# Performance work log

Hardware: AMD Instinct MI355X
Metric: run time of the kernel (lower is better)

The kernel has to match this reference:

```python
import jax, jax.numpy as jnp
import numpy as np

B, N, C = 4, 4096, 128
IK, CK = 9, 9  # inner_k, cross_k
BN_EPS = 1e-5


def setup_inputs() -> dict:
    key = jax.random.key(0)
    ks = jax.random.split(key, 8)
    d = {}
    d["x"] = jax.random.normal(ks[0], (B, N, C), jnp.float32)
    d["y"] = jax.random.normal(ks[1], (B, N, C), jnp.float32)
    d["x_mask"] = jnp.ones((B, N), jnp.float32)
    d["y_mask"] = jnp.ones((B, N), jnp.float32)
    specs = [("mr0", C, 2 * C), ("mr1", C, 2 * C), ("fc", C, C), ("f1", 4 * C, C), ("f2", C, 4 * C)]
    for (name, o, i), k in zip(specs, jax.random.split(ks[2], len(specs))):
        d[name + "_W"] = jax.random.normal(k, (o, i), jnp.float32) * 0.05
        d[name + "_b"] = jnp.zeros((o,), jnp.float32)
        d[name + "_g"] = jnp.ones((o,), jnp.float32)
        d[name + "_beta"] = jnp.zeros((o,), jnp.float32)
        d[name + "_m"] = jnp.zeros((o,), jnp.float32)
        d[name + "_v"] = jnp.ones((o,), jnp.float32)
    return d


def _sqdist(a, b):
    # a: [B,Na,C], b: [B,Nb,C] -> [B,Na,Nb]
    return (jnp.sum(a * a, -1)[:, :, None] + jnp.sum(b * b, -1)[:, None, :]
            - 2.0 * jnp.einsum('bnc,bmc->bnm', a, b))


def _knn(x, y):
    # neighbor indices into concat([x;y]) for every node: [B, Nx+Ny, IK+CK]
    Nx = x.shape[1]
    i_xx = jax.lax.top_k(-_sqdist(x, x), IK)[1]
    i_xy = jax.lax.top_k(-_sqdist(x, y), CK)[1] + Nx
    i_yy = jax.lax.top_k(-_sqdist(y, y), IK)[1] + Nx
    i_yx = jax.lax.top_k(-_sqdist(y, x), CK)[1]
    return jnp.concatenate([jnp.concatenate([i_xx, i_xy], -1),
                            jnp.concatenate([i_yy, i_yx], -1)], axis=1)


def _bn(h, g, b, m, v):
    # eval-mode BatchNorm over channel (last) axis
    return (h - m) * jax.lax.rsqrt(v + BN_EPS) * g + b


def _gelu(h):
    return jax.nn.gelu(h, approximate=False)


def _mrconv(f, nbr, W, b, g, be, m, v):
    # f: [B,Nt,C], nbr: [B,Nt,K] -> Conv(2C->C)+BN+GELU of interleaved [x, max_j(x_j-x_i)]
    xj = jax.vmap(lambda fb, nb: fb[nb])(f, nbr)          # [B,Nt,K,C] gather
    msg = jnp.max(xj - f[:, :, None, :], axis=2)          # [B,Nt,C]
    Bh, Nt, Ch = f.shape
    h = jnp.stack([f, msg], axis=-1).reshape(Bh, Nt, 2 * Ch)  # channel interleave as in torch reshape
    h = jnp.einsum('bnc,oc->bno', h, W) + b
    return _gelu(_bn(h, g, be, m, v))


def _forward(x, x_mask, y, y_mask,
             mr0_W, mr0_b, mr0_g, mr0_beta, mr0_m, mr0_v,
             mr1_W, mr1_b, mr1_g, mr1_beta, mr1_m, mr1_v,
             fc_W, fc_b, fc_g, fc_beta, fc_m, fc_v,
             f1_W, f1_b, f1_g, f1_beta, f1_m, f1_v,
             f2_W, f2_b, f2_g, f2_beta, f2_m, f2_v):
    Nx = x.shape[1]
    nbr = _knn(x, y)
    xy = jnp.concatenate([x, y], axis=1)
    xy = _mrconv(xy, nbr, mr0_W, mr0_b, mr0_g, mr0_beta, mr0_m, mr0_v) + xy
    xy = _mrconv(xy, nbr, mr1_W, mr1_b, mr1_g, mr1_beta, mr1_m, mr1_v) + xy
    xg, yg = xy[:, :Nx], xy[:, Nx:]

    def fc(h):
        return _bn(jnp.einsum('bnc,oc->bno', h, fc_W) + fc_b, fc_g, fc_beta, fc_m, fc_v)

    xo = fc(xg) + x
    yo = fc(yg) + y

    def ffn(h):
        r = h
        h = _gelu(_bn(jnp.einsum('bnc,oc->bno', h, f1_W) + f1_b, f1_g, f1_beta, f1_m, f1_v))
        h = _gelu(_bn(jnp.einsum('bnc,oc->bno', h, f2_W) + f2_b, f2_g, f2_beta, f2_m, f2_v))
        return h + r

    xo = ffn(xo) * x_mask[:, :, None]
    yo = ffn(yo) * y_mask[:, :, None]
    return xo, yo


def reference(x, x_mask, y, y_mask,
              mr0_W, mr0_b, mr0_g, mr0_beta, mr0_m, mr0_v,
              mr1_W, mr1_b, mr1_g, mr1_beta, mr1_m, mr1_v,
              fc_W, fc_b, fc_g, fc_beta, fc_m, fc_v,
              f1_W, f1_b, f1_g, f1_beta, f1_m, f1_v,
              f2_W, f2_b, f2_g, f2_beta, f2_m, f2_v):
    return _forward(x, x_mask, y, y_mask,
                    mr0_W, mr0_b, mr0_g, mr0_beta, mr0_m, mr0_v,
                    mr1_W, mr1_b, mr1_g, mr1_beta, mr1_m, mr1_v,
                    fc_W, fc_b, fc_g, fc_beta, fc_m, fc_v,
                    f1_W, f1_b, f1_g, f1_beta, f1_m, f1_v,
                    f2_W, f2_b, f2_g, f2_beta, f2_m, f2_v)
```

## Files before the change

### kernel.cpp

```cpp
#include <hip/hip_runtime.h>
#include <hip/hip_bf16.h>
#include <float.h>
#include <math.h>

#define BB 4
#define N1 4096
#define NT 8192
#define CH 128
#define NBRS 18
#define ZSEL 2.35f
#define LCAP 40
#define EQ 4096.0f
#define GQGAP 6
#define GQCOV 3

typedef __attribute__((ext_vector_type(8))) short s16x8;
typedef __attribute__((ext_vector_type(16))) float f32x16;
typedef __attribute__((ext_vector_type(4))) float f32x4;

__device__ inline unsigned short f2bf(float v) {
  unsigned u = __float_as_uint(v);
  unsigned r = (u + 0x7FFFu + ((u >> 16) & 1u)) >> 16;
  return (unsigned short)r;
}
__device__ inline float bf2f(unsigned short h) {
  return __uint_as_float((unsigned)h << 16);
}
__device__ inline unsigned mapf(float f) {
  unsigned u = __float_as_uint(f);
  return (u & 0x80000000u) ? ~u : (u | 0x80000000u);
}
__device__ inline float gelu_f(float x) {
  return 0.5f * x * (1.0f + erff(x * 0.70710678118654752f));
}

__global__ __launch_bounds__(256) void wsplit_k(const float* __restrict__ w,
                                                unsigned short* __restrict__ hi,
                                                unsigned short* __restrict__ lo,
                                                int n) {
  int t = blockIdx.x * 256 + threadIdx.x;
  if (t < n) {
    float v = w[t];
    unsigned short h = f2bf(v);
    float r = v - bf2f(h);
    hi[t] = h; lo[t] = f2bf(r);
  }
}

__global__ __launch_bounds__(256) void norms_concat_k(const float* __restrict__ x,
                                                      const float* __restrict__ y,
                                                      float* __restrict__ xy,
                                                      float* __restrict__ norms) {
  int w = (blockIdx.x * 256 + threadIdx.x) >> 6;
  int lane = threadIdx.x & 63;
  int b = w >> 13, row = w & 8191;
  const float* src = (row < N1) ? (x + ((size_t)b * N1 + row) * CH)
                                : (y + ((size_t)b * N1 + (row - N1)) * CH);
  float2 v = *(const float2*)(src + lane * 2);
  *(float2*)(xy + (size_t)w * CH + lane * 2) = v;
  float s = v.x * v.x + v.y * v.y;
  for (int off = 32; off > 0; off >>= 1) s += __shfl_down(s, off);
  if (lane == 0) norms[w] = s;
}

__global__ __launch_bounds__(256) void cbt_k(const float* __restrict__ xy,
                                             unsigned short* __restrict__ cbt) {
  int t = blockIdx.x * 256 + threadIdx.x;
  int u = t >> 15, p = t & 32767;
  const float* src = xy + (size_t)p * CH + u * 8;
  unsigned hw[4], lw[4];
#pragma unroll
  for (int j = 0; j < 4; ++j) {
    float v0 = src[2 * j], v1 = src[2 * j + 1];
    unsigned short h0 = f2bf(v0), h1 = f2bf(v1);
    float r0 = v0 - bf2f(h0);
    float r1 = v1 - bf2f(h1);
    unsigned short l0 = f2bf(r0), l1 = f2bf(r1);
    hw[j] = (unsigned)h0 | ((unsigned)h1 << 16);
    lw[j] = (unsigned)l0 | ((unsigned)l1 << 16);
  }
  *(uint4*)&cbt[((size_t)u * 32768 + p) * 8] = make_uint4(hw[0], hw[1], hw[2], hw[3]);
  *(uint4*)&cbt[((size_t)(u + 16) * 32768 + p) * 8] = make_uint4(lw[0], lw[1], lw[2], lw[3]);
}

__global__ __launch_bounds__(256) void knn4_k(const unsigned short* __restrict__ cbt,
                                              const float* __restrict__ norms,
                                              int* __restrict__ nbr,
                                              int* __restrict__ cntg,
                                              unsigned* __restrict__ listA,
                                              unsigned* __restrict__ listB,
                                              unsigned short* __restrict__ fbl) {
  __shared__ unsigned short __align__(16) cst[2][32][32][8];
  __shared__ float cn_s[2][32];
  __shared__ unsigned lst[128][2][LCAP];
  __shared__ unsigned short lcnt[128][2];
  const int tid = threadIdx.x;
  const int qblk = blockIdx.x, z = blockIdx.y;
  const int b = z >> 2, combo = z & 3;
  const int qoff = (combo <= 1) ? 0 : N1;
  const int coff = (combo == 0 || combo == 3) ? 0 : N1;
  const int w = tid >> 6;
  const int cl = tid & 31;
  const int h = (tid >> 5) & 1;
  const int h4 = 4 * h;
  const int ql = w * 32 + cl;
  const int q = qblk * 128 + ql;
  const size_t qp = (size_t)b * NT + qoff + q;
  const size_t cb0 = (size_t)b * NT + coff;

  const s16x8* cv = (const s16x8*)cbt;
  s16x8 bh[8], bl[8];
#pragma unroll
  for (int s = 0; s < 8; ++s) {
    bh[s] = cv[(size_t)(2 * s + h) * 32768 + qp];
    bl[s] = cv[(size_t)(16 + 2 * s + h) * 32768 + qp];
  }

  const float nq = norms[qp];
  const float Tc = 128.f - ZSEL * sqrtf(256.f + 4.f * nq);
  int cnt = 0;

  const int su = tid >> 5, sc = tid & 31;
  const char* p0 = (const char*)&cbt[((size_t)(su) * 32768 + cb0 + sc) * 8];
  const char* p1 = (const char*)&cbt[((size_t)(8 + su) * 32768 + cb0 + sc) * 8];
  const char* p2 = (const char*)&cbt[((size_t)(16 + su) * 32768 + cb0 + sc) * 8];
  const char* p3 = (const char*)&cbt[((size_t)(24 + su) * 32768 + cb0 + sc) * 8];
  const float* pn = norms + cb0 + tid;

  uint4 st[4]; float cnreg = 0.f;
  st[0] = *(const uint4*)p0; p0 += 512;
  st[1] = *(const uint4*)p1; p1 += 512;
  st[2] = *(const uint4*)p2; p2 += 512;
  st[3] = *(const uint4*)p3; p3 += 512;
  if (tid < 32) { cnreg = *pn; pn += 32; }
  *(uint4*)&cst[0][su][sc][0] = st[0];
  *(uint4*)&cst[0][8 + su][sc][0] = st[1];
  *(uint4*)&cst[0][16 + su][sc][0] = st[2];
  *(uint4*)&cst[0][24 + su][sc][0] = st[3];
  if (tid < 32) cn_s[0][tid] = cnreg;
  __syncthreads();

  int buf = 0;
  for (int t = 0; t < 128; ++t) {
    if (t < 127) {
      st[0] = *(const uint4*)p0; p0 += 512;
      st[1] = *(const uint4*)p1; p1 += 512;
      st[2] = *(const uint4*)p2; p2 += 512;
      st[3] = *(const uint4*)p3; p3 += 512;
      if (tid < 32) { cnreg = *pn; pn += 32; }
    }
    f32x16 acc = {0.f,0.f,0.f,0.f,0.f,0.f,0.f,0.f,0.f,0.f,0.f,0.f,0.f,0.f,0.f,0.f};
#pragma unroll
    for (int s = 0; s < 8; ++s) {
      s16x8 a0 = *(const s16x8*)&cst[buf][2 * s + h][cl][0];
      s16x8 a1 = *(const s16x8*)&cst[buf][16 + 2 * s + h][cl][0];
      acc = __builtin_amdgcn_mfma_f32_32x32x16_bf16(a0, bh[s], acc, 0, 0, 0);
      acc = __builtin_amdgcn_mfma_f32_32x32x16_bf16(a0, bl[s], acc, 0, 0, 0);
      acc = __builtin_amdgcn_mfma_f32_32x32x16_bf16(a1, bh[s], acc, 0, 0, 0);
    }
    float4 c0 = *(const float4*)&cn_s[buf][h4];
    float4 c1 = *(const float4*)&cn_s[buf][8 + h4];
    float4 c2 = *(const float4*)&cn_s[buf][16 + h4];
    float4 c3 = *(const float4*)&cn_s[buf][24 + h4];
    const float cw[16] = {c0.x, c0.y, c0.z, c0.w, c1.x, c1.y, c1.z, c1.w,
                          c2.x, c2.y, c2.z, c2.w, c3.x, c3.y, c3.z, c3.w};
    const int ib = t * 32 + h4;
#pragma unroll
    for (int g = 0; g < 4; ++g) {
#pragma unroll
      for (int rr = 0; rr < 4; ++rr) {
        const int r = g * 4 + rr;
        float s = fmaf(-2.0f, acc[r], cw[r]);
        if (s <= Tc) {
          int e = (int)((Tc - s) * EQ);
          e = e > 0xFFFFF ? 0xFFFFF : e;
          unsigned key = ((unsigned)e << 12) | (unsigned)(4095 - (ib + g * 8 + rr));
          if (cnt < LCAP) lst[ql][h][cnt] = key;
          ++cnt;
        }
      }
    }
    if (t < 127) {
      *(uint4*)&cst[buf ^ 1][su][sc][0] = st[0];
      *(uint4*)&cst[buf ^ 1][8 + su][sc][0] = st[1];
      *(uint4*)&cst[buf ^ 1][16 + su][sc][0] = st[2];
      *(uint4*)&cst[buf ^ 1][24 + su][sc][0] = st[3];
      if (tid < 32) cn_s[buf ^ 1][tid] = cnreg;
    }
    __syncthreads();
    buf ^= 1;
  }
  lcnt[ql][h] = (unsigned short)cnt;
  __syncthreads();

  if (tid < 128) {
    const int mq = tid;
    const int gq = z * 4096 + qblk * 128 + mq;
    const int c0 = lcnt[mq][0], c1 = lcnt[mq][1];
    const bool over = (c0 > LCAP) || (c1 > LCAP);
    const int n0 = c0 > LCAP ? LCAP : c0;
    const int n1 = c1 > LCAP ? LCAP : c1;
    const int m = n0 + n1;
    unsigned top[10];
#pragma unroll
    for (int j = 0; j < 10; ++j) top[j] = 0u;
    for (int li = 0; li < 2; ++li) {
      const int n = li ? n1 : n0;
      for (int i = 0; i < n; ++i) {
        unsigned key = lst[mq][li][i];
        if (key > top[9]) {
#pragma unroll
          for (int j = 0; j < 10; ++j) {
            bool sw = key > top[j];
            unsigned tv = top[j];
            top[j] = sw ? key : tv;
            key = sw ? tv : key;
          }
        }
      }
    }
    const unsigned e8 = top[8] >> 12, e9 = top[9] >> 12;
    const bool cov = !over && (m >= 9) && (e8 >= GQCOV);
    const bool ok = cov && (m == 9 || (e8 - e9) >= GQGAP);
    const int qg = qblk * 128 + mq;
    const int row = (combo <= 1) ? qg : (N1 + qg);
    const int slot = (combo == 0 || combo == 2) ? 0 : 9;
    const int ioff = (combo == 1 || combo == 2) ? N1 : 0;
    int* dst = nbr + ((size_t)b * NT + row) * NBRS + slot;
    if (ok) {
#pragma unroll
      for (int s = 0; s < 9; ++s)
        dst[s] = (int)(4095u - (top[s] & 0xFFFu)) + ioff;
    } else if (!cov || m > 64) {
      int idx = atomicAdd(&cntg[1], 1);
      listB[idx] = (unsigned)gq;
    } else {
      int idx = atomicAdd(&cntg[0], 1);
      listA[idx] = ((unsigned)m << 16) | (unsigned)gq;
      unsigned short* fp = fbl + (size_t)gq * 64;
      int p = 0;
      for (int i = 0; i < n0; ++i) fp[p++] = (unsigned short)(4095u - (lst[mq][0][i] & 0xFFFu));
      for (int i = 0; i < n1; ++i) fp[p++] = (unsigned short)(4095u - (lst[mq][1][i] & 0xFFFu));
    }
  }
}

__global__ __launch_bounds__(256) void rerank_sl_k(const float* __restrict__ xy,
                                                   const float* __restrict__ norms,
                                                   const unsigned short* __restrict__ fbl,
                                                   const unsigned* __restrict__ listA,
                                                   const int* __restrict__ cntg,
                                                   int* __restrict__ nbr) {
  const int lane = threadIdx.x & 63;
  const int wv = threadIdx.x >> 6;
  const int nA = cntg[0];
  for (int i = blockIdx.x * 4 + wv; i < nA; i += gridDim.x * 4) {
    const unsigned ent = listA[i];
    const int gq = (int)(ent & 0xffffu);
    const int m = (int)(ent >> 16);
    const int z = gq >> 12, q = gq & 4095;
    const int b = z >> 2, combo = z & 3;
    const int qoff = (combo <= 1) ? 0 : N1;
    const int coff = (combo == 0 || combo == 3) ? 0 : N1;
    const size_t cq = (size_t)b * NT + coff;
    const int row = (combo <= 1) ? q : (N1 + q);
    const int slot = (combo == 0 || combo == 2) ? 0 : 9;
    const int ioff = (combo == 1 || combo == 2) ? N1 : 0;
    int* dst = nbr + ((size_t)b * NT + row) * NBRS + slot;
    const float* qrow = xy + ((size_t)b * NT + qoff + q) * CH;

    int ci = 0; float de = FLT_MAX;
    if (lane < m) {
      ci = (int)fbl[(size_t)gq * 64 + lane];
      const float* crow = xy + (cq + ci) * CH;
      const float cnv = norms[cq + ci];
      float a0 = 0.f, a1 = 0.f, a2 = 0.f, a3 = 0.f;
#pragma unroll
      for (int k = 0; k < 32; ++k) {
        float4 qv = *(const float4*)(qrow + k * 4);
        float4 cv2 = *(const float4*)(crow + k * 4);
        a0 = fmaf(qv.x, cv2.x, a0); a1 = fmaf(qv.y, cv2.y, a1);
        a2 = fmaf(qv.z, cv2.z, a2); a3 = fmaf(qv.w, cv2.w, a3);
      }
      de = cnv - 2.0f * ((a0 + a1) + (a2 + a3));
    }
    unsigned long long key = ((unsigned long long)mapf(de) << 32) | (unsigned)ci;
    if (lane >= m) key = ~0ull;
    int xr = 0;
#pragma unroll 1
    for (int k = 0; k < m; ++k) {
      unsigned long long kk = __shfl(key, k);
      xr += (kk < key) ? 1 : 0;
    }
    if (lane < m && xr < 9) dst[xr] = ci + ioff;
  }
}

__global__ __launch_bounds__(256) void rerank_fs_k(const float* __restrict__ xy,
                                                   const float* __restrict__ norms,
                                                   const unsigned* __restrict__ listB,
                                                   const int* __restrict__ cntg,
                                                   int* __restrict__ nbr) {
  __shared__ unsigned long long ms[4][576];
  __shared__ unsigned long long wk[36];
  const int tid = threadIdx.x;
  const int lane = tid & 63, wv = tid >> 6;
  const int nB = cntg[1];
  for (int i = blockIdx.x; i < nB; i += gridDim.x) {
    const int gq = (int)listB[i];
    const int z = gq >> 12, q = gq & 4095;
    const int b = z >> 2, combo = z & 3;
    const int qoff = (combo <= 1) ? 0 : N1;
    const int coff = (combo == 0 || combo == 3) ? 0 : N1;
    const size_t cq = (size_t)b * NT + coff;
    const int row = (combo <= 1) ? q : (N1 + q);
    const int slot = (combo == 0 || combo == 2) ? 0 : 9;
    const int ioff = (combo == 1 || combo == 2) ? N1 : 0;
    int* dst = nbr + ((size_t)b * NT + row) * NBRS + slot;
    const float* qrow = xy + ((size_t)b * NT + qoff + q) * CH;

    unsigned long long bl9[9];
#pragma unroll
    for (int j = 0; j < 9; ++j) bl9[j] = ~0ull;
    for (int it = 0; it < 16; ++it) {
      const int cc = (it * 4 + wv) * 64 + lane;
      const float* crow = xy + (cq + cc) * CH;
      float a0 = 0.f, a1 = 0.f, a2 = 0.f, a3 = 0.f;
#pragma unroll
      for (int k = 0; k < 32; ++k) {
        float4 qv = *(const float4*)(qrow + k * 4);
        float4 cv2 = *(const float4*)(crow + k * 4);
        a0 = fmaf(qv.x, cv2.x, a0); a1 = fmaf(qv.y, cv2.y, a1);
        a2 = fmaf(qv.z, cv2.z, a2); a3 = fmaf(qv.w, cv2.w, a3);
      }
      float d2v = norms[cq + cc] - 2.0f * ((a0 + a1) + (a2 + a3));
      unsigned long long key = ((unsigned long long)mapf(d2v) << 32) | (unsigned)cc;
      if (key < bl9[8]) {
#pragma unroll
        for (int jj = 0; jj < 9; ++jj) {
          bool sw = key < bl9[jj];
          unsigned long long tv = bl9[jj];
          bl9[jj] = sw ? key : tv;
          key = sw ? tv : key;
        }
      }
    }
#pragma unroll
    for (int s = 0; s < 9; ++s) ms[wv][lane * 9 + s] = bl9[s];
    int ptr = 0;
    for (int s = 0; s < 9; ++s) {
      unsigned long long hd = ms[wv][lane * 9 + ptr];
      unsigned long long mn = hd;
#pragma unroll
      for (int off = 1; off < 64; off <<= 1) {
        unsigned long long ot = __shfl_xor(mn, off);
        mn = (ot < mn) ? ot : mn;
      }
      unsigned long long wm = __ballot(hd == mn);
      int wl = __ffsll(wm) - 1;
      if (lane == wl) ptr++;
      if (lane == 0) wk[wv * 9 + s] = mn;
    }
    __syncthreads();
    if (wv == 0) {
      unsigned long long key = (lane < 36) ? wk[lane] : ~0ull;
      int xr = 0;
#pragma unroll 1
      for (int k = 0; k < 36; ++k) {
        unsigned long long kk = __shfl(key, k);
        xr += (kk < key) ? 1 : 0;
      }
      if (lane < 36 && xr < 9) dst[xr] = (int)(unsigned)(key & 0xffffffffull) + ioff;
    }
    __syncthreads();
  }
}

__global__ __launch_bounds__(256) void mrconv2_k(const float* __restrict__ in,
                                                 const int* __restrict__ nbr,
                                                 const unsigned short* __restrict__ Whi,
                                                 const unsigned short* __restrict__ Wlo,
                                                 const float* __restrict__ bias,
                                                 const float* __restrict__ gam,
                                                 const float* __restrict__ bet,
                                                 const float* __restrict__ mean,
                                                 const float* __restrict__ var,
                                                 float* __restrict__ out) {
  __shared__ float h[32][260];
  const int tid = threadIdx.x;
  const int pt0 = blockIdx.x * 32;
  {
    const int w = tid >> 6, lane = tid & 63;
    for (int pp = 0; pp < 8; ++pp) {
      const int p = w * 8 + pp;
      const int n = pt0 + p;
      const int b = n >> 13;
      const float* frow = in + (size_t)n * CH;
      float2 f2 = *(const float2*)(frow + lane * 2);
      float mx = -FLT_MAX, my = -FLT_MAX;
      const int* nb = nbr + (size_t)n * NBRS;
      for (int j = 0; j < NBRS; ++j) {
        int idx = nb[j];
        const float* vrow = in + ((size_t)b * NT + idx) * CH;
        float2 v2 = *(const float2*)(vrow + lane * 2);
        mx = fmaxf(mx, v2.x - f2.x);
        my = fmaxf(my, v2.y - f2.y);
      }
      h[p][lane * 4 + 0] = f2.x; h[p][lane * 4 + 1] = mx;
      h[p][lane * 4 + 2] = f2.y; h[p][lane * 4 + 3] = my;
    }
  }
  __syncthreads();
  const int lane = tid & 63, w = tid >> 6;
  const int r16 = lane & 15, kg = lane >> 4;
  f32x4 acc[2][2] = {{{0.f,0.f,0.f,0.f},{0.f,0.f,0.f,0.f}},
                     {{0.f,0.f,0.f,0.f},{0.f,0.f,0.f,0.f}}};
#pragma unroll
  for (int ks = 0; ks < 8; ++ks) {
    s16x8 ah[2], al[2];
#pragma unroll
    for (int rt = 0; rt < 2; ++rt) {
      const float* hp = &h[rt * 16 + r16][(ks * 4 + kg) * 8];
#pragma unroll
      for (int j = 0; j < 8; ++j) {
        float v = hp[j];
        unsigned short hb = f2bf(v);
        float rr = v - bf2f(hb);
        ah[rt][j] = (short)hb;
        al[rt][j] = (short)f2bf(rr);
      }
    }
#pragma unroll
    for (int cbi = 0; cbi < 2; ++cbi) {
      const int o = (w * 2 + cbi) * 16 + r16;
      s16x8 bh2 = *(const s16x8*)(Whi + o * 256 + ks * 32 + kg * 8);
      s16x8 bl2 = *(const s16x8*)(Wlo + o * 256 + ks * 32 + kg * 8);
#pragma unroll
      for (int rt = 0; rt < 2; ++rt) {
        acc[rt][cbi] = __builtin_amdgcn_mfma_f32_16x16x32_bf16(ah[rt], bh2, acc[rt][cbi], 0, 0, 0);
        acc[rt][cbi] = __builtin_amdgcn_mfma_f32_16x16x32_bf16(ah[rt], bl2, acc[rt][cbi], 0, 0, 0);
        acc[rt][cbi] = __builtin_amdgcn_mfma_f32_16x16x32_bf16(al[rt], bh2, acc[rt][cbi], 0, 0, 0);
      }
    }
  }
#pragma unroll
  for (int cbi = 0; cbi < 2; ++cbi) {
    const int o = (w * 2 + cbi) * 16 + r16;
    const float sc = gam[o] / sqrtf(var[o] + 1e-5f);
    const float bs = bias[o], mo = mean[o], be = bet[o];
#pragma unroll
    for (int rt = 0; rt < 2; ++rt) {
#pragma unroll
      for (int rg = 0; rg < 4; ++rg) {
        const int row = rt * 16 + kg * 4 + rg;
        const int n = pt0 + row;
        float bn = (acc[rt][cbi][rg] + bs - mo) * sc + be;
        float gl = gelu_f(bn);
        out[(size_t)n * CH + o] = gl + h[row][2 * o];
      }
    }
  }
}

__global__ __launch_bounds__(256) void fc2_k(const float* __restrict__ in,
                                             const unsigned short* __restrict__ Whi,
                                             const unsigned short* __restrict__ Wlo,
                                             const float* __restrict__ bias,
                                             const float* __restrict__ gam,
                                             const float* __restrict__ bet,
                                             const float* __restrict__ mean,
                                             const float* __restrict__ var,
                                             const float* __restrict__ xres,
                                             const float* __restrict__ yres,
                                             float* __restrict__ out) {
  __shared__ unsigned short __align__(16) aHi[16][16][8];
  __shared__ unsigned short __align__(16) aLo[16][16][8];
  const int tid = threadIdx.x;
  const int pt0 = blockIdx.x * 16;
  {
    const int row = tid >> 4, ku = tid & 15;
    const float* src = in + (size_t)(pt0 + row) * CH + ku * 8;
    unsigned hw[4], lw[4];
#pragma unroll
    for (int j = 0; j < 4; ++j) {
      float v0 = src[2 * j], v1 = src[2 * j + 1];
      unsigned short h0 = f2bf(v0), h1 = f2bf(v1);
      float r0 = v0 - bf2f(h0), r1 = v1 - bf2f(h1);
      hw[j] = (unsigned)h0 | ((unsigned)h1 << 16);
      lw[j] = (unsigned)f2bf(r0) | ((unsigned)f2bf(r1) << 16);
    }
    *(uint4*)&aHi[ku][row][0] = make_uint4(hw[0], hw[1], hw[2], hw[3]);
    *(uint4*)&aLo[ku][row][0] = make_uint4(lw[0], lw[1], lw[2], lw[3]);
  }
  __syncthreads();
  const int lane = tid & 63, w = tid >> 6;
  const int r16 = lane & 15, kg = lane >> 4;
  f32x4 acc[2] = {{0.f,0.f,0.f,0.f}, {0.f,0.f,0.f,0.f}};
#pragma unroll
  for (int ks = 0; ks < 4; ++ks) {
    s16x8 ah = *(const s16x8*)&aHi[ks * 4 + kg][r16][0];
    s16x8 al = *(const s16x8*)&aLo[ks * 4 + kg][r16][0];
#pragma unroll
    for (int cb = 0; cb < 2; ++cb) {
      const int o = w * 32 + cb * 16 + r16;
      s16x8 bh2 = *(const s16x8*)(Whi + o * 128 + ks * 32 + kg * 8);
      s16x8 bl2 = *(const s16x8*)(Wlo + o * 128 + ks * 32 + kg * 8);
      acc[cb] = __builtin_amdgcn_mfma_f32_16x16x32_bf16(ah, bh2, acc[cb], 0, 0, 0);
      acc[cb] = __builtin_amdgcn_mfma_f32_16x16x32_bf16(ah, bl2, acc[cb], 0, 0, 0);
      acc[cb] = __builtin_amdgcn_mfma_f32_16x16x32_bf16(al, bh2, acc[cb], 0, 0, 0);
    }
  }
#pragma unroll
  for (int cb = 0; cb < 2; ++cb) {
    const int o = w * 32 + cb * 16 + r16;
    const float sc = gam[o] / sqrtf(var[o] + 1e-5f);
    const float bs = bias[o], mo = mean[o], be = bet[o];
#pragma unroll
    for (int rg = 0; rg < 4; ++rg) {
      const int row = kg * 4 + rg;
      const int n = pt0 + row;
      const int b = n >> 13, prow = n & 8191;
      float bn = (acc[cb][rg] + bs - mo) * sc + be;
      float res = (prow < N1) ? xres[((size_t)b * N1 + prow) * CH + o]
                              : yres[((size_t)b * N1 + prow - N1) * CH + o];
      out[(size_t)n * CH + o] = bn + res;
    }
  }
}

__global__ __launch_bounds__(256) void ffn2_k(const float* __restrict__ u,
                                              const unsigned short* __restrict__ W1hi,
                                              const unsigned short* __restrict__ W1lo,
                                              const float* __restrict__ b1,
                                              const float* __restrict__ g1,
                                              const float* __restrict__ be1,
                                              const float* __restrict__ m1,
                                              const float* __restrict__ v1,
                                              const unsigned short* __restrict__ W2hi,
                                              const unsigned short* __restrict__ W2lo,
                                              const float* __restrict__ b2,
                                              const float* __restrict__ g2,
                                              const float* __restrict__ be2,
                                              const float* __restrict__ m2,
                                              const float* __restrict__ v2,
                                              const float* __restrict__ xmask,
                                              const float* __restrict__ ymask,
                                              float* __restrict__ outbuf) {
  __shared__ unsigned short __align__(16) aHi[16][16][8];
  __shared__ unsigned short __align__(16) aLo[16][16][8];
  __shared__ unsigned short __align__(16) hHi[64][16][8];
  __shared__ unsigned short __align__(16) hLo[64][16][8];
  const int tid = threadIdx.x;
  const int pt0 = blockIdx.x * 16;
  {
    const int row = tid >> 4, ku = tid & 15;
    const float* src = u + (size_t)(pt0 + row) * CH + ku * 8;
    unsigned hw[4], lw[4];
#pragma unroll
    for (int j = 0; j < 4; ++j) {
      float v0 = src[2 * j], v1 = src[2 * j + 1];
      unsigned short h0 = f2bf(v0), h1 = f2bf(v1);
      float r0 = v0 - bf2f(h0), r1 = v1 - bf2f(h1);
      hw[j] = (unsigned)h0 | ((unsigned)h1 << 16);
      lw[j] = (unsigned)f2bf(r0) | ((unsigned)f2bf(r1) << 16);
    }
    *(uint4*)&aHi[ku][row][0] = make_uint4(hw[0], hw[1], hw[2], hw[3]);
    *(uint4*)&aLo[ku][row][0] = make_uint4(lw[0], lw[1], lw[2], lw[3]);
  }
  __syncthreads();
  const int lane = tid & 63, w = tid >> 6;
  const int r16 = lane & 15, kg = lane >> 4;
  {
    f32x4 acc[8];
#pragma unroll
    for (int cb = 0; cb < 8; ++cb) acc[cb] = {0.f, 0.f, 0.f, 0.f};
#pragma unroll
    for (int ks = 0; ks < 4; ++ks) {
      s16x8 ah = *(const s16x8*)&aHi[ks * 4 + kg][r16][0];
      s16x8 al = *(const s16x8*)&aLo[ks * 4 + kg][r16][0];
#pragma unroll
      for (int cb = 0; cb < 8; ++cb) {
        const int o = w * 128 + cb * 16 + r16;
        s16x8 bh2 = *(const s16x8*)(W1hi + o * 128 + ks * 32 + kg * 8);
        s16x8 bl2 = *(const s16x8*)(W1lo + o * 128 + ks * 32 + kg * 8);
        acc[cb] = __builtin_amdgcn_mfma_f32_16x16x32_bf16(ah, bh2, acc[cb], 0, 0, 0);
        acc[cb] = __builtin_amdgcn_mfma_f32_16x16x32_bf16(ah, bl2, acc[cb], 0, 0, 0);
        acc[cb] = __builtin_amdgcn_mfma_f32_16x16x32_bf16(al, bh2, acc[cb], 0, 0, 0);
      }
    }
#pragma unroll
    for (int cb = 0; cb < 8; ++cb) {
      const int o = w * 128 + cb * 16 + r16;
      const float sc = g1[o] / sqrtf(v1[o] + 1e-5f);
      const float bs = b1[o], mo = m1[o], be = be1[o];
#pragma unroll
      for (int rg = 0; rg < 4; ++rg) {
        const int row = kg * 4 + rg;
        float bn = (acc[cb][rg] + bs - mo) * sc + be;
        float gl = gelu_f(bn);
        unsigned short hb = f2bf(gl);
        float rr = gl - bf2f(hb);
        hHi[o >> 3][row][o & 7] = hb;
        hLo[o >> 3][row][o & 7] = f2bf(rr);
      }
    }
  }
  __syncthreads();
  {
    f32x4 acc[2] = {{0.f,0.f,0.f,0.f}, {0.f,0.f,0.f,0.f}};
#pragma unroll
    for (int ks = 0; ks < 16; ++ks) {
      s16x8 ah = *(const s16x8*)&hHi[ks * 4 + kg][r16][0];
      s16x8 al = *(const s16x8*)&hLo[ks * 4 + kg][r16][0];
#pragma unroll
      for (int cb = 0; cb < 2; ++cb) {
        const int o = w * 32 + cb * 16 + r16;
        s16x8 bh2 = *(const s16x8*)(W2hi + o * 512 + ks * 32 + kg * 8);
        s16x8 bl2 = *(const s16x8*)(W2lo + o * 512 + ks * 32 + kg * 8);
        acc[cb] = __builtin_amdgcn_mfma_f32_16x16x32_bf16(ah, bh2, acc[cb], 0, 0, 0);
        acc[cb] = __builtin_amdgcn_mfma_f32_16x16x32_bf16(ah, bl2, acc[cb], 0, 0, 0);
        acc[cb] = __builtin_amdgcn_mfma_f32_16x16x32_bf16(al, bh2, acc[cb], 0, 0, 0);
      }
    }
#pragma unroll
    for (int cb = 0; cb < 2; ++cb) {
      const int o = w * 32 + cb * 16 + r16;
      const float sc = g2[o] / sqrtf(v2[o] + 1e-5f);
      const float bs = b2[o], mo = m2[o], be = be2[o];
#pragma unroll
      for (int rg = 0; rg < 4; ++rg) {
        const int row = kg * 4 + rg;
        const int n = pt0 + row;
        const int b = n >> 13, prow = n & 8191;
        float bn = (acc[cb][rg] + bs - mo) * sc + be;
        float gl = gelu_f(bn);
        float res = u[(size_t)n * CH + o];
        float msk; size_t oidx;
        if (prow < N1) {
          msk = xmask[(size_t)b * N1 + prow];
          oidx = ((size_t)b * N1 + prow) * CH + o;
        } else {
          msk = ymask[(size_t)b * N1 + prow - N1];
          oidx = (size_t)BB * N1 * CH + ((size_t)b * N1 + prow - N1) * CH + o;
        }
        outbuf[oidx] = (gl + res) * msk;
      }
    }
  }
}

extern "C" void kernel_launch(void* const* d_in, const int* in_sizes, int n_in,
                              void* d_out, int out_size, void* d_ws, size_t ws_size,
                              hipStream_t stream) {
  const float* x  = (const float*)d_in[0];
  const float* y  = (const float*)d_in[1];
  const float* xm = (const float*)d_in[2];
  const float* ym = (const float*)d_in[3];
  const float* mr0W = (const float*)d_in[4];
  const float* mr1W = (const float*)d_in[10];
  const float* fcW  = (const float*)d_in[16];
  const float* f1W  = (const float*)d_in[22];
  const float* f2W  = (const float*)d_in[28];

  char* ws = (char*)d_ws;
  float*          xyA   = (float*)(ws + 0);
  unsigned short* cbt   = (unsigned short*)(ws + 16777216);
  float*          xyB   = (float*)(ws + 16777216);
  float*          norms = (float*)(ws + 33554432);
  int*            cntg  = (int*)(ws + 33685504);
  unsigned*       listA = (unsigned*)(ws + 33689600);
  unsigned*       listB = (unsigned*)(ws + 33951744);
  unsigned short* fbl   = (unsigned short*)(ws + 34213888);
  int*            nbr   = (int*)(ws + 42602496);
  unsigned short* mr0hi = (unsigned short*)(ws + 44961792);
  unsigned short* mr0lo = (unsigned short*)(ws + 45027328);
  unsigned short* mr1hi = (unsigned short*)(ws + 45092864);
  unsigned short* mr1lo = (unsigned short*)(ws + 45158400);
  unsigned short* fcWhi = (unsigned short*)(ws + 45223936);
  unsigned short* fcWlo = (unsigned short*)(ws + 45256704);
  unsigned short* f1hi  = (unsigned short*)(ws + 45289472);
  unsigned short* f1lo  = (unsigned short*)(ws + 45420544);
  unsigned short* f2hi  = (unsigned short*)(ws + 45551616);
  unsigned short* f2lo  = (unsigned short*)(ws + 45682688);

  hipMemsetAsync(cntg, 0, 8, stream);

  wsplit_k<<<128, 256, 0, stream>>>(mr0W, mr0hi, mr0lo, 128 * 256);
  wsplit_k<<<128, 256, 0, stream>>>(mr1W, mr1hi, mr1lo, 128 * 256);
  wsplit_k<<<64, 256, 0, stream>>>(fcW, fcWhi, fcWlo, 128 * 128);
  wsplit_k<<<256, 256, 0, stream>>>(f1W, f1hi, f1lo, 512 * 128);
  wsplit_k<<<256, 256, 0, stream>>>(f2W, f2hi, f2lo, 128 * 512);

  norms_concat_k<<<8192, 256, 0, stream>>>(x, y, xyA, norms);
  cbt_k<<<2048, 256, 0, stream>>>(xyA, cbt);
  knn4_k<<<dim3(32, 16), 256, 0, stream>>>(cbt, norms, nbr, cntg, listA, listB, fbl);
  rerank_sl_k<<<256, 256, 0, stream>>>(xyA, norms, fbl, listA, cntg, nbr);
  rerank_fs_k<<<256, 256, 0, stream>>>(xyA, norms, listB, cntg, nbr);

  mrconv2_k<<<1024, 256, 0, stream>>>(xyA, nbr, mr0hi, mr0lo,
      (const float*)d_in[5], (const float*)d_in[6], (const float*)d_in[7],
      (const float*)d_in[8], (const float*)d_in[9], xyB);
  mrconv2_k<<<1024, 256, 0, stream>>>(xyB, nbr, mr1hi, mr1lo,
      (const float*)d_in[11], (const float*)d_in[12], (const float*)d_in[13],
      (const float*)d_in[14], (const float*)d_in[15], xyA);

  fc2_k<<<2048, 256, 0, stream>>>(xyA, fcWhi, fcWlo,
      (const float*)d_in[17], (const float*)d_in[18], (const float*)d_in[19],
      (const float*)d_in[20], (const float*)d_in[21], x, y, xyB);

  ffn2_k<<<2048, 256, 0, stream>>>(xyB,
      f1hi, f1lo, (const float*)d_in[23], (const float*)d_in[24], (const float*)d_in[25],
      (const float*)d_in[26], (const float*)d_in[27],
      f2hi, f2lo, (const float*)d_in[29], (const float*)d_in[30], (const float*)d_in[31],
      (const float*)d_in[32], (const float*)d_in[33],
      xm, ym, (float*)d_out);
}
```

Before: 576.1 us.

## Keep per-thread register top-12 in kNN instead of shared candidate lists

The kNN kernel now keeps each thread's candidates in a 12-entry sorted register list via compare-swap insertion, replacing the 40-entry shared-memory list per query half. The two half-lists are merged at the end through a dump into the reused tile buffer. A new safety check on the smallest kept key decides between the short rerank path and the full-scan fallback. The fallback candidate buffer shrinks from 64 to 24 entries. This removes a large shared-memory footprint, which may raise occupancy, and cuts the serial merge work. The cost is more registers and extra VALU work for every insertion.

```diff
diff --git a/kernel.cpp b/kernel.cpp
--- a/kernel.cpp
+++ b/kernel.cpp
@@ -9,7 +9,6 @@
 #define CH 128
 #define NBRS 18
 #define ZSEL 2.35f
-#define LCAP 40
 #define EQ 4096.0f
 #define GQGAP 6
 #define GQCOV 3
@@ -33,6 +32,18 @@
 __device__ inline float gelu_f(float x) {
   return 0.5f * x * (1.0f + erff(x * 0.70710678118654752f));
 }
+
+#define INS12U(l, key0)                         \
+  {                                             \
+    unsigned nk = key0;                         \
+    _Pragma("unroll")                           \
+    for (int j = 0; j < 12; ++j) {              \
+      bool sw = nk > l[j];                      \
+      unsigned tv = l[j];                       \
+      l[j] = sw ? nk : tv;                      \
+      nk = sw ? tv : nk;                        \
+    }                                           \
+  }
 
 __global__ __launch_bounds__(256) void wsplit_k(const float* __restrict__ w,
                                                 unsigned short* __restrict__ hi,
@@ -83,7 +94,7 @@
   *(uint4*)&cbt[((size_t)(u + 16) * 32768 + p) * 8] = make_uint4(lw[0], lw[1], lw[2], lw[3]);
 }
 
-__global__ __launch_bounds__(256) void knn4_k(const unsigned short* __restrict__ cbt,
+__global__ __launch_bounds__(256) void knn9_k(const unsigned short* __restrict__ cbt,
                                               const float* __restrict__ norms,
                                               int* __restrict__ nbr,
                                               int* __restrict__ cntg,
@@ -92,8 +103,7 @@
                                               unsigned short* __restrict__ fbl) {
   __shared__ unsigned short __align__(16) cst[2][32][32][8];
   __shared__ float cn_s[2][32];
-  __shared__ unsigned lst[128][2][LCAP];
-  __shared__ unsigned short lcnt[128][2];
+  __shared__ unsigned short cnt2[128][2];
   const int tid = threadIdx.x;
   const int qblk = blockIdx.x, z = blockIdx.y;
   const int b = z >> 2, combo = z & 3;
@@ -119,6 +129,9 @@
   const float nq = norms[qp];
   const float Tc = 128.f - ZSEL * sqrtf(256.f + 4.f * nq);
   int cnt = 0;
+  unsigned lA[12];
+#pragma unroll
+  for (int j = 0; j < 12; ++j) lA[j] = 0u;
 
   const int su = tid >> 5, sc = tid & 31;
   const char* p0 = (const char*)&cbt[((size_t)(su) * 32768 + cb0 + sc) * 8];
@@ -166,18 +179,15 @@
                           c2.x, c2.y, c2.z, c2.w, c3.x, c3.y, c3.z, c3.w};
     const int ib = t * 32 + h4;
 #pragma unroll
-    for (int g = 0; g < 4; ++g) {
-#pragma unroll
-      for (int rr = 0; rr < 4; ++rr) {
-        const int r = g * 4 + rr;
-        float s = fmaf(-2.0f, acc[r], cw[r]);
-        if (s <= Tc) {
-          int e = (int)((Tc - s) * EQ);
-          e = e > 0xFFFFF ? 0xFFFFF : e;
-          unsigned key = ((unsigned)e << 12) | (unsigned)(4095 - (ib + g * 8 + rr));
-          if (cnt < LCAP) lst[ql][h][cnt] = key;
-          ++cnt;
-        }
+    for (int r = 0; r < 16; ++r) {
+      const int idx = ib + (r & 3) + 8 * (r >> 2);
+      float s = fmaf(-2.0f, acc[r], cw[r]);
+      if (s <= Tc) {
+        ++cnt;
+        int e = (int)((Tc - s) * EQ);
+        e = e > 0xFFFFF ? 0xFFFFF : e;
+        unsigned key = ((unsigned)e << 12) | (unsigned)(4095 - idx);
+        if (key > lA[11]) INS12U(lA, key);
       }
     }
     if (t < 127) {
@@ -190,57 +200,57 @@
     __syncthreads();
     buf ^= 1;
   }
-  lcnt[ql][h] = (unsigned short)cnt;
+
+  unsigned* dmp = (unsigned*)&cst[0][0][0][0];
+#pragma unroll
+  for (int j = 0; j < 12; ++j) dmp[((size_t)ql * 2 + h) * 12 + j] = lA[j];
+  cnt2[ql][h] = (unsigned short)(cnt > 65535 ? 65535 : cnt);
   __syncthreads();
 
   if (tid < 128) {
     const int mq = tid;
     const int gq = z * 4096 + qblk * 128 + mq;
-    const int c0 = lcnt[mq][0], c1 = lcnt[mq][1];
-    const bool over = (c0 > LCAP) || (c1 > LCAP);
-    const int n0 = c0 > LCAP ? LCAP : c0;
-    const int n1 = c1 > LCAP ? LCAP : c1;
-    const int m = n0 + n1;
-    unsigned top[10];
-#pragma unroll
-    for (int j = 0; j < 10; ++j) top[j] = 0u;
-    for (int li = 0; li < 2; ++li) {
-      const int n = li ? n1 : n0;
-      for (int i = 0; i < n; ++i) {
-        unsigned key = lst[mq][li][i];
-        if (key > top[9]) {
-#pragma unroll
-          for (int j = 0; j < 10; ++j) {
-            bool sw = key > top[j];
-            unsigned tv = top[j];
-            top[j] = sw ? key : tv;
-            key = sw ? tv : key;
-          }
-        }
-      }
-    }
-    const unsigned e8 = top[8] >> 12, e9 = top[9] >> 12;
-    const bool cov = !over && (m >= 9) && (e8 >= GQCOV);
-    const bool ok = cov && (m == 9 || (e8 - e9) >= GQGAP);
+    const int c0 = cnt2[mq][0], c1 = cnt2[mq][1];
+    const int k0 = c0 > 12 ? 12 : c0, k1 = c1 > 12 ? 12 : c1;
+    const int m_true = c0 + c1;
+    const unsigned* pa = &dmp[((size_t)mq * 2 + 0) * 12];
+    const unsigned* pb = &dmp[((size_t)mq * 2 + 1) * 12];
+    unsigned mg[10];
+    int i = 0, j = 0;
+#pragma unroll
+    for (int s = 0; s < 10; ++s) {
+      unsigned av = pa[i], bv = pb[j];
+      bool ta = av >= bv;
+      mg[s] = ta ? av : bv;
+      if (ta) ++i; else ++j;
+    }
+    const unsigned e8 = mg[8] >> 12, e9 = mg[9] >> 12;
+    const bool cov = (m_true >= 9) && (e8 >= GQCOV);
+    const bool gapok = (m_true == 9) || ((e8 - e9) >= GQGAP);
+    unsigned emink = 0xFFFFFFFFu;
+    if (c0 > 12) emink = pa[11] >> 12;
+    if (c1 > 12) { unsigned e = pb[11] >> 12; if (e < emink) emink = e; }
+    const bool slok = (emink == 0xFFFFFFFFu) || (emink + 6 <= e8);
+
     const int qg = qblk * 128 + mq;
     const int row = (combo <= 1) ? qg : (N1 + qg);
     const int slot = (combo == 0 || combo == 2) ? 0 : 9;
     const int ioff = (combo == 1 || combo == 2) ? N1 : 0;
     int* dst = nbr + ((size_t)b * NT + row) * NBRS + slot;
-    if (ok) {
+    if (cov && gapok) {
 #pragma unroll
       for (int s = 0; s < 9; ++s)
-        dst[s] = (int)(4095u - (top[s] & 0xFFFu)) + ioff;
-    } else if (!cov || m > 64) {
+        dst[s] = (int)(4095u - (mg[s] & 0xFFFu)) + ioff;
+    } else if (!cov || !slok) {
       int idx = atomicAdd(&cntg[1], 1);
       listB[idx] = (unsigned)gq;
     } else {
       int idx = atomicAdd(&cntg[0], 1);
-      listA[idx] = ((unsigned)m << 16) | (unsigned)gq;
-      unsigned short* fp = fbl + (size_t)gq * 64;
+      listA[idx] = ((unsigned)(k0 + k1) << 16) | (unsigned)gq;
+      unsigned short* fp = fbl + (size_t)gq * 24;
       int p = 0;
-      for (int i = 0; i < n0; ++i) fp[p++] = (unsigned short)(4095u - (lst[mq][0][i] & 0xFFFu));
-      for (int i = 0; i < n1; ++i) fp[p++] = (unsigned short)(4095u - (lst[mq][1][i] & 0xFFFu));
+      for (int t2 = 0; t2 < k0; ++t2) fp[p++] = (unsigned short)(4095u - (pa[t2] & 0xFFFu));
+      for (int t2 = 0; t2 < k1; ++t2) fp[p++] = (unsigned short)(4095u - (pb[t2] & 0xFFFu));
     }
   }
 }
@@ -271,7 +281,7 @@
 
     int ci = 0; float de = FLT_MAX;
     if (lane < m) {
-      ci = (int)fbl[(size_t)gq * 64 + lane];
+      ci = (int)fbl[(size_t)gq * 24 + lane];
       const float* crow = xy + (cq + ci) * CH;
       const float cnv = norms[cq + ci];
       float a0 = 0.f, a1 = 0.f, a2 = 0.f, a3 = 0.f;
@@ -671,17 +681,17 @@
   unsigned*       listA = (unsigned*)(ws + 33689600);
   unsigned*       listB = (unsigned*)(ws + 33951744);
   unsigned short* fbl   = (unsigned short*)(ws + 34213888);
-  int*            nbr   = (int*)(ws + 42602496);
-  unsigned short* mr0hi = (unsigned short*)(ws + 44961792);
-  unsigned short* mr0lo = (unsigned short*)(ws + 45027328);
-  unsigned short* mr1hi = (unsigned short*)(ws + 45092864);
-  unsigned short* mr1lo = (unsigned short*)(ws + 45158400);
-  unsigned short* fcWhi = (unsigned short*)(ws + 45223936);
-  unsigned short* fcWlo = (unsigned short*)(ws + 45256704);
-  unsigned short* f1hi  = (unsigned short*)(ws + 45289472);
-  unsigned short* f1lo  = (unsigned short*)(ws + 45420544);
-  unsigned short* f2hi  = (unsigned short*)(ws + 45551616);
-  unsigned short* f2lo  = (unsigned short*)(ws + 45682688);
+  int*            nbr   = (int*)(ws + 37359616);
+  unsigned short* mr0hi = (unsigned short*)(ws + 39718912);
+  unsigned short* mr0lo = (unsigned short*)(ws + 39784448);
+  unsigned short* mr1hi = (unsigned short*)(ws + 39849984);
+  unsigned short* mr1lo = (unsigned short*)(ws + 39915520);
+  unsigned short* fcWhi = (unsigned short*)(ws + 39981056);
+  unsigned short* fcWlo = (unsigned short*)(ws + 40013824);
+  unsigned short* f1hi  = (unsigned short*)(ws + 40046592);
+  unsigned short* f1lo  = (unsigned short*)(ws + 40177664);
+  unsigned short* f2hi  = (unsigned short*)(ws + 40308736);
+  unsigned short* f2lo  = (unsigned short*)(ws + 40439808);
 
   hipMemsetAsync(cntg, 0, 8, stream);
 
@@ -693,7 +703,7 @@
 
   norms_concat_k<<<8192, 256, 0, stream>>>(x, y, xyA, norms);
   cbt_k<<<2048, 256, 0, stream>>>(xyA, cbt);
-  knn4_k<<<dim3(32, 16), 256, 0, stream>>>(cbt, norms, nbr, cntg, listA, listB, fbl);
+  knn9_k<<<dim3(32, 16), 256, 0, stream>>>(cbt, norms, nbr, cntg, listA, listB, fbl);
   rerank_sl_k<<<256, 256, 0, stream>>>(xyA, norms, fbl, listA, cntg, nbr);
   rerank_fs_k<<<256, 256, 0, stream>>>(xyA, norms, listB, cntg, nbr);
 
```

Measured after the change: 607.7 us. 1.05x slower.
